# Kernel tuning notes

Hardware: AMD Instinct MI355X
Metric: run time of the kernel (lower is better)

The kernel has to match this reference:

```python
import jax, jax.numpy as jnp
import numpy as np

S, D, H = 4096, 2048, 16
HD = D // H

def setup_inputs() -> dict:
    key = jax.random.key(0)
    ks = jax.random.split(key, 9)
    s = 1.0 / np.sqrt(D)
    return {
        "hidden_states": jax.random.normal(ks[0], (S, D), jnp.float32),
        "Wq": jax.random.uniform(ks[1], (D, D), jnp.float32, -s, s),
        "bq": jax.random.uniform(ks[2], (D,), jnp.float32, -s, s),
        "Wk": jax.random.uniform(ks[3], (D, D), jnp.float32, -s, s),
        "bk": jax.random.uniform(ks[4], (D,), jnp.float32, -s, s),
        "Wv": jax.random.uniform(ks[5], (D, D), jnp.float32, -s, s),
        "bv": jax.random.uniform(ks[6], (D,), jnp.float32, -s, s),
        "Wo": jax.random.uniform(ks[7], (D, D), jnp.float32, -s, s),
        "bo": jax.random.uniform(ks[8], (D,), jnp.float32, -s, s),
    }

def reference(hidden_states, Wq, bq, Wk, bk, Wv, bv, Wo, bo):
    seq = hidden_states.shape[0]
    # projections (torch Linear: x @ W.T + b)
    q = (hidden_states @ Wq.T + bq).reshape(seq, H, HD).transpose(1, 0, 2)  # [H,S,hd]
    k = (hidden_states @ Wk.T + bk).reshape(seq, H, HD).transpose(1, 0, 2)
    v = (hidden_states @ Wv.T + bv).reshape(seq, H, HD).transpose(1, 0, 2)
    scale = 1.0 / np.sqrt(HD).astype(np.float32)
    qk = jnp.einsum('hqd,hkd->hqk', q, k) * scale  # [H,S,S]
    causal = jnp.tril(jnp.ones((seq, seq), bool))
    qk = jnp.where(causal, qk, -jnp.inf)
    attn = jax.nn.softmax(qk, axis=-1)
    out = jnp.einsum('hqk,hkd->hqd', attn, v)  # [H,S,hd]
    out = out.transpose(1, 0, 2).reshape(seq, D)
    return out @ Wo.T + bo
```

## Files before the change

kernel.cpp:

```cpp
#include <hip/hip_runtime.h>
#include <stdint.h>

#define S_LEN 4096
#define D_DIM 2048
#define NHEAD 16
#define HDIM  128

typedef short bf16x8 __attribute__((ext_vector_type(8)));
typedef float f32x4  __attribute__((ext_vector_type(4)));
typedef float f32x16 __attribute__((ext_vector_type(16)));

__device__ __forceinline__ unsigned short f2bf(float x) {
  union { float f; unsigned u; } v; v.f = x;
  unsigned r = v.u + 0x7FFFu + ((v.u >> 16) & 1u);
  return (unsigned short)(r >> 16);
}

__device__ __forceinline__ float bf2f(unsigned short s) {
  union { unsigned u; float f; } v; v.u = ((unsigned)s) << 16;
  return v.f;
}

__device__ __forceinline__ unsigned cvtpk_bf16(float lo, float hi_) {
  unsigned r;
  asm("v_cvt_pk_bf16_f32 %0, %1, %2" : "=v"(r) : "v"(lo), "v"(hi_));
  return r;
}

__device__ __forceinline__ void gload_lds16(const void* g, void* l) {
  __builtin_amdgcn_global_load_lds(
      (const __attribute__((address_space(1))) unsigned int*)g,
      (__attribute__((address_space(3))) unsigned int*)l, 16, 0, 0);
}

__global__ __launch_bounds__(256) void cvt_all(
    const float* __restrict__ X, const float* __restrict__ Wq,
    const float* __restrict__ Wk, const float* __restrict__ Wv,
    const float* __restrict__ Wo, unsigned short* __restrict__ out) {
  const size_t DD = (size_t)D_DIM * D_DIM;
  size_t i = ((size_t)blockIdx.x * 256 + threadIdx.x) * 8;
  const float* src; size_t off;
  if (i < 2 * DD)      { src = X;  off = i; }
  else if (i < 3 * DD) { src = Wq; off = i - 2 * DD; }
  else if (i < 4 * DD) { src = Wk; off = i - 3 * DD; }
  else if (i < 5 * DD) { src = Wv; off = i - 4 * DD; }
  else                 { src = Wo; off = i - 5 * DD; }
  float4 a = *(const float4*)(src + off);
  float4 b = *(const float4*)(src + off + 4);
  union { unsigned short s[8]; bf16x8 v; } o;
  o.s[0] = f2bf(a.x); o.s[1] = f2bf(a.y); o.s[2] = f2bf(a.z); o.s[3] = f2bf(a.w);
  o.s[4] = f2bf(b.x); o.s[5] = f2bf(b.y); o.s[6] = f2bf(b.z); o.s[7] = f2bf(b.w);
  *(bf16x8*)(out + i) = o.v;
}

__device__ __forceinline__ void stage_ab(
    const unsigned short* __restrict__ A, const unsigned short* __restrict__ W,
    unsigned short* la, unsigned short* lb, int m0, int n0, int k0,
    int wv, int lane) {
  const int K = 2048;
#pragma unroll
  for (int p = 0; p < 4; ++p) {
    const int off = wv * 1024 + p * 8192;
    const int o = off + lane * 16;
    const int row = o >> 7, ch = (o >> 4) & 7;
    const int csrc = (ch ^ (row & 7)) * 8;
    gload_lds16(A + (size_t)(m0 + row) * K + k0 + csrc, la + (off >> 1));
  }
#pragma unroll
  for (int p = 0; p < 3; ++p) {
    const int off = wv * 1024 + p * 8192;
    const int o = off + lane * 16;
    const int row = o >> 7, ch = (o >> 4) & 7;
    const int csrc = (ch ^ (row & 7)) * 8;
    gload_lds16(W + (size_t)(n0 + row) * K + k0 + csrc, lb + (off >> 1));
  }
}

__global__ __launch_bounds__(512, 1) void gemm_qkv2(
    const unsigned short* __restrict__ A, const unsigned short* __restrict__ W,
    const float* __restrict__ bq, const float* __restrict__ bk,
    const float* __restrict__ bv, unsigned short* __restrict__ Q,
    unsigned short* __restrict__ Ko, unsigned short* __restrict__ V,
    float qsc) {
  __shared__ __attribute__((aligned(16))) unsigned short LA[2][16384];
  __shared__ __attribute__((aligned(16))) unsigned short LB[2][12288];
  const int m0 = blockIdx.y * 256, n0 = blockIdx.x * 192;
  const int tid = threadIdx.x, lane = tid & 63, wv = tid >> 6;
  const int wm = wv >> 2, wn = wv & 3;
  const int rA = lane & 15, g4 = lane >> 4;

  f32x4 acc[8][3];
#pragma unroll
  for (int i = 0; i < 8; ++i)
#pragma unroll
    for (int j = 0; j < 3; ++j)
#pragma unroll
      for (int r = 0; r < 4; ++r) acc[i][j][r] = 0.f;

  stage_ab(A, W, &LA[0][0], &LB[0][0], m0, n0, 0, wv, lane);
  stage_ab(A, W, &LA[1][0], &LB[1][0], m0, n0, 64, wv, lane);
  asm volatile("s_waitcnt vmcnt(7)" ::: "memory");
  __builtin_amdgcn_s_barrier();
  __builtin_amdgcn_sched_barrier(0);

  for (int t = 0; t < 32; ++t) {
    const unsigned short* la = &LA[t & 1][0];
    const unsigned short* lb = &LB[t & 1][0];
#pragma unroll
    for (int kk = 0; kk < 2; ++kk) {
      bf16x8 af[8], bfv[3];
      const int sw = ((kk * 4 + g4) ^ (rA & 7)) * 8;
#pragma unroll
      for (int i = 0; i < 8; ++i)
        af[i] = *(const bf16x8*)(la + (wm * 128 + i * 16 + rA) * 64 + sw);
#pragma unroll
      for (int j = 0; j < 3; ++j)
        bfv[j] = *(const bf16x8*)(lb + (wn * 48 + j * 16 + rA) * 64 + sw);
      __builtin_amdgcn_s_setprio(1);
#pragma unroll
      for (int i = 0; i < 8; ++i)
#pragma unroll
        for (int j = 0; j < 3; ++j)
          acc[i][j] = __builtin_amdgcn_mfma_f32_16x16x32_bf16(af[i], bfv[j], acc[i][j], 0, 0, 0);
      __builtin_amdgcn_s_setprio(0);
    }
    if (t == 31) break;
    __builtin_amdgcn_s_barrier();
    __builtin_amdgcn_sched_barrier(0);
    if (t + 2 < 32) {
      stage_ab(A, W, &LA[t & 1][0], &LB[t & 1][0], m0, n0, (t + 2) * 64, wv, lane);
      asm volatile("s_waitcnt vmcnt(7)" ::: "memory");
    } else {
      asm volatile("s_waitcnt vmcnt(0)" ::: "memory");
    }
    __builtin_amdgcn_s_barrier();
    __builtin_amdgcn_sched_barrier(0);
  }

  const int cR = g4 * 4, cC = rA;
#pragma unroll
  for (int j = 0; j < 3; ++j) {
    const int colb = n0 + wn * 48 + j * 16;
    const int seg = colb >> 11, clb = colb & 2047;
    const float* bp = (seg == 0) ? bq : (seg == 1) ? bk : bv;
    unsigned short* op = (seg == 0) ? Q : (seg == 1) ? Ko : V;
    const float es = (seg == 0) ? qsc : 1.0f;
    const int cl = clb + cC;
    const float bvv = bp[cl];
#pragma unroll
    for (int i = 0; i < 8; ++i) {
      const int row0 = m0 + wm * 128 + i * 16 + cR;
#pragma unroll
      for (int r = 0; r < 4; ++r)
        op[(size_t)(row0 + r) * D_DIM + cl] = f2bf((acc[i][j][r] + bvv) * es);
    }
  }
}

__device__ __forceinline__ void stage_o(
    const unsigned short* __restrict__ A, const unsigned short* __restrict__ W,
    unsigned short* la, unsigned short* lb, int m0, int n0, int k0,
    int wv, int lane) {
#pragma unroll
  for (int p = 0; p < 4; ++p) {
    const int off = wv * 1024 + p * 8192;
    const int o = off + lane * 16;
    const int row = o >> 7, ch = (o >> 4) & 7;
    gload_lds16(A + (size_t)(m0 + row) * 2048 + k0 + ((ch ^ (row & 7)) << 3),
                la + (off >> 1));
  }
#pragma unroll
  for (int p = 0; p < 2; ++p) {
    const int off = wv * 1024 + p * 8192;
    const int o = off + lane * 16;
    const int row = o >> 7, ch = (o >> 4) & 7;
    gload_lds16(W + (size_t)(n0 + row) * 2048 + k0 + ((ch ^ (row & 7)) << 3),
                lb + (off >> 1));
  }
}

__global__ __launch_bounds__(512, 1) void gemm_o256(
    const unsigned short* __restrict__ A, const unsigned short* __restrict__ W,
    const float* __restrict__ bias, float* __restrict__ Cout) {
  __shared__ __attribute__((aligned(16))) unsigned short LA[2][16384];
  __shared__ __attribute__((aligned(16))) unsigned short LB[2][8192];
  const int m0 = blockIdx.y * 256, n0 = blockIdx.x * 128;
  const int tid = threadIdx.x, lane = tid & 63, wv = tid >> 6;
  const int wm = wv >> 2, wn = wv & 3;
  const int rA = lane & 15, g4 = lane >> 4;

  f32x4 acc[8][2];
#pragma unroll
  for (int i = 0; i < 8; ++i)
#pragma unroll
    for (int j = 0; j < 2; ++j)
#pragma unroll
      for (int r = 0; r < 4; ++r) acc[i][j][r] = 0.f;

  stage_o(A, W, &LA[0][0], &LB[0][0], m0, n0, 0, wv, lane);
  stage_o(A, W, &LA[1][0], &LB[1][0], m0, n0, 64, wv, lane);
  asm volatile("s_waitcnt vmcnt(6)" ::: "memory");
  __builtin_amdgcn_s_barrier();
  __builtin_amdgcn_sched_barrier(0);

  for (int t = 0; t < 32; ++t) {
    const unsigned short* la = &LA[t & 1][0];
    const unsigned short* lb = &LB[t & 1][0];
#pragma unroll
    for (int kk = 0; kk < 2; ++kk) {
      bf16x8 af[8], bfv[2];
      const int sw = ((kk * 4 + g4) ^ (rA & 7)) * 8;
#pragma unroll
      for (int i = 0; i < 8; ++i)
        af[i] = *(const bf16x8*)(la + (wm * 128 + i * 16 + rA) * 64 + sw);
#pragma unroll
      for (int j = 0; j < 2; ++j)
        bfv[j] = *(const bf16x8*)(lb + (wn * 32 + j * 16 + rA) * 64 + sw);
      __builtin_amdgcn_s_setprio(1);
#pragma unroll
      for (int i = 0; i < 8; ++i)
#pragma unroll
        for (int j = 0; j < 2; ++j)
          acc[i][j] = __builtin_amdgcn_mfma_f32_16x16x32_bf16(af[i], bfv[j], acc[i][j], 0, 0, 0);
      __builtin_amdgcn_s_setprio(0);
    }
    if (t == 31) break;
    __builtin_amdgcn_s_barrier();
    __builtin_amdgcn_sched_barrier(0);
    if (t + 2 < 32) {
      stage_o(A, W, &LA[t & 1][0], &LB[t & 1][0], m0, n0, (t + 2) * 64, wv, lane);
      asm volatile("s_waitcnt vmcnt(6)" ::: "memory");
    } else {
      asm volatile("s_waitcnt vmcnt(0)" ::: "memory");
    }
    __builtin_amdgcn_s_barrier();
    __builtin_amdgcn_sched_barrier(0);
  }

  const int cR = g4 * 4, cC = rA;
#pragma unroll
  for (int j = 0; j < 2; ++j) {
    const int col = n0 + wn * 32 + j * 16 + cC;
    const float bvv = bias[col];
#pragma unroll
    for (int i = 0; i < 8; ++i) {
      const int row0 = m0 + wm * 128 + i * 16 + cR;
#pragma unroll
      for (int r = 0; r < 4; ++r)
        Cout[(size_t)(row0 + r) * D_DIM + col] = acc[i][j][r] + bvv;
    }
  }
}

__global__ __launch_bounds__(256, 2) void attn_part(
    const unsigned short* __restrict__ Qb, const unsigned short* __restrict__ Kb,
    const unsigned short* __restrict__ Vb, unsigned short* __restrict__ Opart,
    float* __restrict__ ML) {
  __shared__ __attribute__((aligned(16))) unsigned short Ks[64 * 128];
  __shared__ __attribute__((aligned(16))) unsigned short Vt[128 * 64];
  const int bid = blockIdx.x;
  const int h  = ((bid & 7) << 1) | ((bid >> 3) & 1);
  const int hf = (bid >> 4) & 1;
  const int qi = 31 - (bid >> 5);
  const int q0 = qi * 128;
  const int u2 = (h * 32 + qi) * 2 + hf;
  const int tid = threadIdx.x, lane = tid & 63, wv = tid >> 6;
  const int qc = lane & 31, hi = lane >> 5;
  const int q0w = q0 + wv * 32;
  const int myq = q0w + qc;
  const int kp = tid & 31, hb = (tid >> 5) * 16;

  bf16x8 qf[8];
#pragma unroll
  for (int sl = 0; sl < 8; ++sl)
    qf[sl] = *(const bf16x8*)(Qb + (size_t)myq * D_DIM + h * HDIM + sl * 16 + hi * 8);

  f32x16 oacc[4];
#pragma unroll
  for (int nf = 0; nf < 4; ++nf)
#pragma unroll
    for (int r = 0; r < 16; ++r) oacc[nf][r] = 0.f;
  float mh = -3.0e38f, l = 0.f;

  const int klo = hf * (qi + 1), khi = klo + qi + 1;
  const int wqmax = q0w + 31;

  for (int kt = klo; kt < khi; ++kt) {
    const int k0 = kt * 64;
    union { uint4 u[4]; unsigned short s[32]; } t;
    {
      const unsigned short* s0 = Vb + (size_t)(k0 + 2 * kp) * D_DIM + h * HDIM + hb;
      t.u[0] = *(const uint4*)s0;           t.u[1] = *(const uint4*)(s0 + 8);
      t.u[2] = *(const uint4*)(s0 + D_DIM); t.u[3] = *(const uint4*)(s0 + D_DIM + 8);
    }
    __syncthreads();
#pragma unroll
    for (int p = 0; p < 4; ++p) {
      const int ob = wv * 4096 + p * 1024;
      const int o = ob + lane * 16;
      const int r = o >> 8, c = (o >> 4) & 15;
      gload_lds16(Kb + (size_t)(k0 + r) * D_DIM + h * HDIM + (c ^ (r & 7)) * 8,
                  Ks + ob / 2);
    }
#pragma unroll
    for (int w = 0; w < 16; ++w) {
      const int hd = hb + w;
      const unsigned val = (unsigned)t.s[w] | ((unsigned)t.s[16 + w] << 16);
      *(unsigned*)((char*)Vt + hd * 128 + (((kp >> 2) ^ (hd & 7)) << 4) + ((kp & 3) << 2)) = val;
    }
    __syncthreads();
    if (k0 > wqmax) continue;

    f32x16 sacc[2];
#pragma unroll
    for (int kb = 0; kb < 2; ++kb)
#pragma unroll
      for (int r = 0; r < 16; ++r) sacc[kb][r] = 0.f;
    __builtin_amdgcn_s_setprio(1);
#pragma unroll
    for (int sl = 0; sl < 8; ++sl) {
#pragma unroll
      for (int kb = 0; kb < 2; ++kb) {
        const int row = kb * 32 + qc;
        bf16x8 kfr = *(const bf16x8*)((const char*)Ks + row * 256 +
                                      (((2 * sl + hi) ^ (qc & 7)) << 4));
        sacc[kb] = __builtin_amdgcn_mfma_f32_32x32x16_bf16(kfr, qf[sl], sacc[kb], 0, 0, 0);
      }
    }
    __builtin_amdgcn_s_setprio(0);

    const bool needmask = (k0 + 63 > q0w);
    if (needmask) {
      const int dq = myq - k0;
#pragma unroll
      for (int kb = 0; kb < 2; ++kb)
#pragma unroll
        for (int r = 0; r < 16; ++r) {
          const int kk = kb * 32 + (r & 3) + 8 * (r >> 2) + 4 * hi;
          if (kk > dq) sacc[kb][r] = -3.0e38f;
        }
    }
    float mx0[8];
#pragma unroll
    for (int tx = 0; tx < 8; ++tx)
      mx0[tx] = fmaxf(fmaxf(sacc[0][tx], sacc[0][tx + 8]),
                      fmaxf(sacc[1][tx], sacc[1][tx + 8]));
    float mx = fmaxf(fmaxf(fmaxf(mx0[0], mx0[1]), fmaxf(mx0[2], mx0[3])),
                     fmaxf(fmaxf(mx0[4], mx0[5]), fmaxf(mx0[6], mx0[7])));
    mx = fmaxf(mx, __shfl_xor(mx, 32));
    if (!__all(mx <= mh + 11.5f)) {
      const float mnew = fmaxf(mh, mx);
      const float corr = exp2f(mh - mnew);
      mh = mnew;
      l *= corr;
#pragma unroll
      for (int r = 0; r < 16; ++r) {
        const float cr = __shfl(corr, (r & 3) + 8 * (r >> 2) + 4 * hi);
#pragma unroll
        for (int nf = 0; nf < 4; ++nf) oacc[nf][r] *= cr;
      }
    }
    float rs = 0.f;
#pragma unroll
    for (int kb = 0; kb < 2; ++kb)
#pragma unroll
      for (int r = 0; r < 16; ++r) {
        const float p = exp2f(sacc[kb][r] - mh);
        sacc[kb][r] = p;
        rs += p;
      }
    rs += __shfl_xor(rs, 32);
    l += rs;

    bf16x8 pa[4];
#pragma unroll
    for (int kb = 0; kb < 2; ++kb)
#pragma unroll
      for (int s = 0; s < 2; ++s) {
        const int b = s * 8;
        unsigned pk0 = cvtpk_bf16(sacc[kb][b + 0], sacc[kb][b + 1]);
        unsigned pk1 = cvtpk_bf16(sacc[kb][b + 2], sacc[kb][b + 3]);
        unsigned pk2 = cvtpk_bf16(sacc[kb][b + 4], sacc[kb][b + 5]);
        unsigned pk3 = cvtpk_bf16(sacc[kb][b + 6], sacc[kb][b + 7]);
        const unsigned sw0 = (unsigned)__shfl_xor((int)pk0, 32);
        const unsigned sw1 = (unsigned)__shfl_xor((int)pk1, 32);
        const unsigned sw2 = (unsigned)__shfl_xor((int)pk2, 32);
        const unsigned sw3 = (unsigned)__shfl_xor((int)pk3, 32);
        union { unsigned u[4]; bf16x8 v; } f;
        if (hi) { f.u[0] = sw2; f.u[1] = sw3; f.u[2] = pk2; f.u[3] = pk3; }
        else    { f.u[0] = pk0; f.u[1] = pk1; f.u[2] = sw0; f.u[3] = sw1; }
        pa[kb * 2 + s] = f.v;
      }

    __builtin_amdgcn_s_setprio(1);
#pragma unroll
    for (int nf = 0; nf < 4; ++nf) {
      const int hd = 32 * nf + qc;
#pragma unroll
      for (int ks = 0; ks < 4; ++ks) {
        bf16x8 vf = *(const bf16x8*)((const char*)Vt + hd * 128 +
                                     (((2 * ks + hi) ^ (qc & 7)) << 4));
        oacc[nf] = __builtin_amdgcn_mfma_f32_32x32x16_bf16(pa[ks], vf, oacc[nf], 0, 0, 0);
      }
    }
    __builtin_amdgcn_s_setprio(0);
  }

  unsigned short* ob = Opart + (size_t)u2 * 16384;
#pragma unroll
  for (int r = 0; r < 16; ++r) {
    const int rl = wv * 32 + (r & 3) + 8 * (r >> 2) + 4 * hi;
#pragma unroll
    for (int nf = 0; nf < 4; ++nf)
      ob[rl * 128 + 32 * nf + qc] = f2bf(oacc[nf][r]);
  }
  if (hi == 0) {
    ML[(size_t)u2 * 256 + wv * 32 + qc] = mh;
    ML[(size_t)u2 * 256 + 128 + wv * 32 + qc] = l;
  }
}

__global__ __launch_bounds__(256) void attn_combine(
    const unsigned short* __restrict__ Opart, const float* __restrict__ ML,
    unsigned short* __restrict__ Ob) {
  const int u = blockIdx.x;
  const int h = u >> 5, qi = u & 31;
  const int tid = threadIdx.x;
  const int row = tid >> 1, c0 = (tid & 1) * 64;
  const float m1 = ML[(size_t)(u * 2 + 0) * 256 + row];
  const float l1 = ML[(size_t)(u * 2 + 0) * 256 + 128 + row];
  const float m2 = ML[(size_t)(u * 2 + 1) * 256 + row];
  const float l2 = ML[(size_t)(u * 2 + 1) * 256 + 128 + row];
  const float M  = fmaxf(m1, m2);
  const float a1 = exp2f(m1 - M), a2 = exp2f(m2 - M);
  const float inv = 1.f / (a1 * l1 + a2 * l2);
  const unsigned short* p1 = Opart + (size_t)(u * 2 + 0) * 16384 + row * 128 + c0;
  const unsigned short* p2 = Opart + (size_t)(u * 2 + 1) * 16384 + row * 128 + c0;
  unsigned short* o = Ob + (size_t)(qi * 128 + row) * D_DIM + h * HDIM + c0;
#pragma unroll
  for (int c = 0; c < 64; c += 8) {
    bf16x8 v1 = *(const bf16x8*)(p1 + c);
    bf16x8 v2 = *(const bf16x8*)(p2 + c);
    union { unsigned short s[8]; bf16x8 v; } out;
#pragma unroll
    for (int e = 0; e < 8; ++e)
      out.s[e] = f2bf((bf2f((unsigned short)v1[e]) * a1 +
                       bf2f((unsigned short)v2[e]) * a2) * inv);
    *(bf16x8*)(o + c) = out.v;
  }
}

extern "C" void kernel_launch(void* const* d_in, const int* in_sizes, int n_in,
                              void* d_out, int out_size, void* d_ws, size_t ws_size,
                              hipStream_t stream) {
  const float* X  = (const float*)d_in[0];
  const float* Wq = (const float*)d_in[1];
  const float* bq = (const float*)d_in[2];
  const float* Wk = (const float*)d_in[3];
  const float* bk = (const float*)d_in[4];
  const float* Wv = (const float*)d_in[5];
  const float* bv = (const float*)d_in[6];
  const float* Wo = (const float*)d_in[7];
  const float* bo = (const float*)d_in[8];
  float* out = (float*)d_out;

  unsigned short* ws = (unsigned short*)d_ws;
  const size_t SD = (size_t)S_LEN * D_DIM;
  const size_t DD = (size_t)D_DIM * D_DIM;
  unsigned short* Xb  = ws;
  unsigned short* Wqb = Xb + SD;
  unsigned short* Wob = Wqb + 3 * DD;
  unsigned short* Qb  = Wob + DD;
  unsigned short* Kb  = Qb + SD;
  unsigned short* Vb  = Kb + SD;
  unsigned short* AOb = Vb + SD;
  unsigned short* Opart = ws;
  float* ML = (float*)(ws + SD + 2 * DD);

  cvt_all<<<(int)(6 * DD / 8 / 256), 256, 0, stream>>>(X, Wq, Wk, Wv, Wo, Xb);

  const float qsc = 0.08838834764831845f * 1.4426950408889634f;
  gemm_qkv2<<<dim3(32, 16), 512, 0, stream>>>(Xb, Wqb, bq, bk, bv, Qb, Kb, Vb, qsc);

  attn_part<<<dim3(1024), 256, 0, stream>>>(Qb, Kb, Vb, Opart, ML);
  attn_combine<<<dim3(512), 256, 0, stream>>>(Opart, ML, AOb);

  gemm_o256<<<dim3(16, 16), 512, 0, stream>>>(AOb, Wob, bo, out);
}
```

Measured before the change: 318.8 us.

## Load two 64-key tiles per barrier pair in attention partial kernel

The attention key loop now stages two 64-row K/V tiles (128 keys) into doubled shared-memory buffers per iteration, then processes both sub-tiles before the next sync. This halves the number of __syncthreads pairs and global-load phases per block, letting more memory traffic be in flight at once. It doubles LDS use to 64KB per block, which may limit occupancy to fewer blocks per CU despite launch_bounds(256,2).

```diff
diff --git a/kernel.cpp b/kernel.cpp
--- a/kernel.cpp
+++ b/kernel.cpp
@@ -256,8 +256,8 @@
     const unsigned short* __restrict__ Qb, const unsigned short* __restrict__ Kb,
     const unsigned short* __restrict__ Vb, unsigned short* __restrict__ Opart,
     float* __restrict__ ML) {
-  __shared__ __attribute__((aligned(16))) unsigned short Ks[64 * 128];
-  __shared__ __attribute__((aligned(16))) unsigned short Vt[128 * 64];
+  __shared__ __attribute__((aligned(16))) unsigned short Ks[128 * 128];
+  __shared__ __attribute__((aligned(16))) unsigned short Vt[128 * 128];
   const int bid = blockIdx.x;
   const int h  = ((bid & 7) << 1) | ((bid >> 3) & 1);
   const int hf = (bid >> 4) & 1;
@@ -285,125 +285,154 @@
   const int klo = hf * (qi + 1), khi = klo + qi + 1;
   const int wqmax = q0w + 31;
 
-  for (int kt = klo; kt < khi; ++kt) {
-    const int k0 = kt * 64;
-    union { uint4 u[4]; unsigned short s[32]; } t;
+  for (int ktp = klo; ktp < khi; ktp += 2) {
+    const int k0 = ktp * 64;
+    const int nsub2 = ((khi - ktp) >= 2) ? 1 : 0;
+    union { uint4 u[4]; unsigned short s[32]; } t0;
     {
       const unsigned short* s0 = Vb + (size_t)(k0 + 2 * kp) * D_DIM + h * HDIM + hb;
-      t.u[0] = *(const uint4*)s0;           t.u[1] = *(const uint4*)(s0 + 8);
-      t.u[2] = *(const uint4*)(s0 + D_DIM); t.u[3] = *(const uint4*)(s0 + D_DIM + 8);
+      t0.u[0] = *(const uint4*)s0;           t0.u[1] = *(const uint4*)(s0 + 8);
+      t0.u[2] = *(const uint4*)(s0 + D_DIM); t0.u[3] = *(const uint4*)(s0 + D_DIM + 8);
     }
     __syncthreads();
 #pragma unroll
     for (int p = 0; p < 4; ++p) {
-      const int ob = wv * 4096 + p * 1024;
+      const int ob = (p * 4 + wv) * 1024;
       const int o = ob + lane * 16;
       const int r = o >> 8, c = (o >> 4) & 15;
       gload_lds16(Kb + (size_t)(k0 + r) * D_DIM + h * HDIM + (c ^ (r & 7)) * 8,
                   Ks + ob / 2);
     }
+    if (nsub2) {
+#pragma unroll
+      for (int p = 4; p < 8; ++p) {
+        const int ob = (p * 4 + wv) * 1024;
+        const int o = ob + lane * 16;
+        const int r = o >> 8, c = (o >> 4) & 15;
+        gload_lds16(Kb + (size_t)(k0 + r) * D_DIM + h * HDIM + (c ^ (r & 7)) * 8,
+                    Ks + ob / 2);
+      }
+    }
 #pragma unroll
     for (int w = 0; w < 16; ++w) {
       const int hd = hb + w;
-      const unsigned val = (unsigned)t.s[w] | ((unsigned)t.s[16 + w] << 16);
-      *(unsigned*)((char*)Vt + hd * 128 + (((kp >> 2) ^ (hd & 7)) << 4) + ((kp & 3) << 2)) = val;
+      const unsigned val = (unsigned)t0.s[w] | ((unsigned)t0.s[16 + w] << 16);
+      *(unsigned*)((char*)Vt + hd * 256 + (((kp >> 2) ^ (hd & 7)) << 4) + ((kp & 3) << 2)) = val;
+    }
+    if (nsub2) {
+      union { uint4 u[4]; unsigned short s[32]; } t1;
+      const unsigned short* s1 = Vb + (size_t)(k0 + 64 + 2 * kp) * D_DIM + h * HDIM + hb;
+      t1.u[0] = *(const uint4*)s1;           t1.u[1] = *(const uint4*)(s1 + 8);
+      t1.u[2] = *(const uint4*)(s1 + D_DIM); t1.u[3] = *(const uint4*)(s1 + D_DIM + 8);
+#pragma unroll
+      for (int w = 0; w < 16; ++w) {
+        const int hd = hb + w;
+        const unsigned val = (unsigned)t1.s[w] | ((unsigned)t1.s[16 + w] << 16);
+        *(unsigned*)((char*)Vt + hd * 256 + (((8 + (kp >> 2)) ^ (hd & 7)) << 4) + ((kp & 3) << 2)) = val;
+      }
     }
     __syncthreads();
-    if (k0 > wqmax) continue;
-
-    f32x16 sacc[2];
-#pragma unroll
-    for (int kb = 0; kb < 2; ++kb)
-#pragma unroll
-      for (int r = 0; r < 16; ++r) sacc[kb][r] = 0.f;
-    __builtin_amdgcn_s_setprio(1);
-#pragma unroll
-    for (int sl = 0; sl < 8; ++sl) {
-#pragma unroll
-      for (int kb = 0; kb < 2; ++kb) {
-        const int row = kb * 32 + qc;
-        bf16x8 kfr = *(const bf16x8*)((const char*)Ks + row * 256 +
-                                      (((2 * sl + hi) ^ (qc & 7)) << 4));
-        sacc[kb] = __builtin_amdgcn_mfma_f32_32x32x16_bf16(kfr, qf[sl], sacc[kb], 0, 0, 0);
+
+#pragma unroll
+    for (int s = 0; s < 2; ++s) {
+      if (s == 1 && !nsub2) break;
+      const int k0s = k0 + s * 64;
+      if (k0s > wqmax) continue;
+
+      f32x16 sacc[2];
+#pragma unroll
+      for (int kb = 0; kb < 2; ++kb)
+#pragma unroll
+        for (int r = 0; r < 16; ++r) sacc[kb][r] = 0.f;
+      __builtin_amdgcn_s_setprio(1);
+#pragma unroll
+      for (int sl = 0; sl < 8; ++sl) {
+#pragma unroll
+        for (int kb = 0; kb < 2; ++kb) {
+          const int row = s * 64 + kb * 32 + qc;
+          bf16x8 kfr = *(const bf16x8*)((const char*)Ks + row * 256 +
+                                        (((2 * sl + hi) ^ (qc & 7)) << 4));
+          sacc[kb] = __builtin_amdgcn_mfma_f32_32x32x16_bf16(kfr, qf[sl], sacc[kb], 0, 0, 0);
+        }
       }
-    }
-    __builtin_amdgcn_s_setprio(0);
-
-    const bool needmask = (k0 + 63 > q0w);
-    if (needmask) {
-      const int dq = myq - k0;
+      __builtin_amdgcn_s_setprio(0);
+
+      const bool needmask = (k0s + 63 > q0w);
+      if (needmask) {
+        const int dq = myq - k0s;
+#pragma unroll
+        for (int kb = 0; kb < 2; ++kb)
+#pragma unroll
+          for (int r = 0; r < 16; ++r) {
+            const int kk = kb * 32 + (r & 3) + 8 * (r >> 2) + 4 * hi;
+            if (kk > dq) sacc[kb][r] = -3.0e38f;
+          }
+      }
+      float mx0[8];
+#pragma unroll
+      for (int tx = 0; tx < 8; ++tx)
+        mx0[tx] = fmaxf(fmaxf(sacc[0][tx], sacc[0][tx + 8]),
+                        fmaxf(sacc[1][tx], sacc[1][tx + 8]));
+      float mx = fmaxf(fmaxf(fmaxf(mx0[0], mx0[1]), fmaxf(mx0[2], mx0[3])),
+                       fmaxf(fmaxf(mx0[4], mx0[5]), fmaxf(mx0[6], mx0[7])));
+      mx = fmaxf(mx, __shfl_xor(mx, 32));
+      if (!__all(mx <= mh + 11.5f)) {
+        const float mnew = fmaxf(mh, mx);
+        const float corr = exp2f(mh - mnew);
+        mh = mnew;
+        l *= corr;
+#pragma unroll
+        for (int r = 0; r < 16; ++r) {
+          const float cr = __shfl(corr, (r & 3) + 8 * (r >> 2) + 4 * hi);
+#pragma unroll
+          for (int nf = 0; nf < 4; ++nf) oacc[nf][r] *= cr;
+        }
+      }
+      float rs = 0.f;
 #pragma unroll
       for (int kb = 0; kb < 2; ++kb)
 #pragma unroll
         for (int r = 0; r < 16; ++r) {
-          const int kk = kb * 32 + (r & 3) + 8 * (r >> 2) + 4 * hi;
-          if (kk > dq) sacc[kb][r] = -3.0e38f;
+          const float p = exp2f(sacc[kb][r] - mh);
+          sacc[kb][r] = p;
+          rs += p;
         }
-    }
-    float mx0[8];
-#pragma unroll
-    for (int tx = 0; tx < 8; ++tx)
-      mx0[tx] = fmaxf(fmaxf(sacc[0][tx], sacc[0][tx + 8]),
-                      fmaxf(sacc[1][tx], sacc[1][tx + 8]));
-    float mx = fmaxf(fmaxf(fmaxf(mx0[0], mx0[1]), fmaxf(mx0[2], mx0[3])),
-                     fmaxf(fmaxf(mx0[4], mx0[5]), fmaxf(mx0[6], mx0[7])));
-    mx = fmaxf(mx, __shfl_xor(mx, 32));
-    if (!__all(mx <= mh + 11.5f)) {
-      const float mnew = fmaxf(mh, mx);
-      const float corr = exp2f(mh - mnew);
-      mh = mnew;
-      l *= corr;
-#pragma unroll
-      for (int r = 0; r < 16; ++r) {
-        const float cr = __shfl(corr, (r & 3) + 8 * (r >> 2) + 4 * hi);
-#pragma unroll
-        for (int nf = 0; nf < 4; ++nf) oacc[nf][r] *= cr;
+      rs += __shfl_xor(rs, 32);
+      l += rs;
+
+      bf16x8 pa[4];
+#pragma unroll
+      for (int kb = 0; kb < 2; ++kb)
+#pragma unroll
+        for (int sx = 0; sx < 2; ++sx) {
+          const int b = sx * 8;
+          unsigned pk0 = cvtpk_bf16(sacc[kb][b + 0], sacc[kb][b + 1]);
+          unsigned pk1 = cvtpk_bf16(sacc[kb][b + 2], sacc[kb][b + 3]);
+          unsigned pk2 = cvtpk_bf16(sacc[kb][b + 4], sacc[kb][b + 5]);
+          unsigned pk3 = cvtpk_bf16(sacc[kb][b + 6], sacc[kb][b + 7]);
+          const unsigned sw0 = (unsigned)__shfl_xor((int)pk0, 32);
+          const unsigned sw1 = (unsigned)__shfl_xor((int)pk1, 32);
+          const unsigned sw2 = (unsigned)__shfl_xor((int)pk2, 32);
+          const unsigned sw3 = (unsigned)__shfl_xor((int)pk3, 32);
+          union { unsigned u[4]; bf16x8 v; } f;
+          if (hi) { f.u[0] = sw2; f.u[1] = sw3; f.u[2] = pk2; f.u[3] = pk3; }
+          else    { f.u[0] = pk0; f.u[1] = pk1; f.u[2] = sw0; f.u[3] = sw1; }
+          pa[kb * 2 + sx] = f.v;
+        }
+
+      __builtin_amdgcn_s_setprio(1);
+#pragma unroll
+      for (int nf = 0; nf < 4; ++nf) {
+        const int hd = 32 * nf + qc;
+#pragma unroll
+        for (int ks = 0; ks < 4; ++ks) {
+          bf16x8 vf = *(const bf16x8*)((const char*)Vt + hd * 256 +
+                                       ((((s << 3) + 2 * ks + hi) ^ (hd & 7)) << 4));
+          oacc[nf] = __builtin_amdgcn_mfma_f32_32x32x16_bf16(pa[ks], vf, oacc[nf], 0, 0, 0);
+        }
       }
-    }
-    float rs = 0.f;
-#pragma unroll
-    for (int kb = 0; kb < 2; ++kb)
-#pragma unroll
-      for (int r = 0; r < 16; ++r) {
-        const float p = exp2f(sacc[kb][r] - mh);
-        sacc[kb][r] = p;
-        rs += p;
-      }
-    rs += __shfl_xor(rs, 32);
-    l += rs;
-
-    bf16x8 pa[4];
-#pragma unroll
-    for (int kb = 0; kb < 2; ++kb)
-#pragma unroll
-      for (int s = 0; s < 2; ++s) {
-        const int b = s * 8;
-        unsigned pk0 = cvtpk_bf16(sacc[kb][b + 0], sacc[kb][b + 1]);
-        unsigned pk1 = cvtpk_bf16(sacc[kb][b + 2], sacc[kb][b + 3]);
-        unsigned pk2 = cvtpk_bf16(sacc[kb][b + 4], sacc[kb][b + 5]);
-        unsigned pk3 = cvtpk_bf16(sacc[kb][b + 6], sacc[kb][b + 7]);
-        const unsigned sw0 = (unsigned)__shfl_xor((int)pk0, 32);
-        const unsigned sw1 = (unsigned)__shfl_xor((int)pk1, 32);
-        const unsigned sw2 = (unsigned)__shfl_xor((int)pk2, 32);
-        const unsigned sw3 = (unsigned)__shfl_xor((int)pk3, 32);
-        union { unsigned u[4]; bf16x8 v; } f;
-        if (hi) { f.u[0] = sw2; f.u[1] = sw3; f.u[2] = pk2; f.u[3] = pk3; }
-        else    { f.u[0] = pk0; f.u[1] = pk1; f.u[2] = sw0; f.u[3] = sw1; }
-        pa[kb * 2 + s] = f.v;
-      }
-
-    __builtin_amdgcn_s_setprio(1);
-#pragma unroll
-    for (int nf = 0; nf < 4; ++nf) {
-      const int hd = 32 * nf + qc;
-#pragma unroll
-      for (int ks = 0; ks < 4; ++ks) {
-        bf16x8 vf = *(const bf16x8*)((const char*)Vt + hd * 128 +
-                                     (((2 * ks + hi) ^ (qc & 7)) << 4));
-        oacc[nf] = __builtin_amdgcn_mfma_f32_32x32x16_bf16(pa[ks], vf, oacc[nf], 0, 0, 0);
-      }
-    }
-    __builtin_amdgcn_s_setprio(0);
+      __builtin_amdgcn_s_setprio(0);
+    }
   }
 
   unsigned short* ob = Opart + (size_t)u2 * 16384;
```

Measured after the change: 319.6 us. About the same (+0.3%).
